# Performance work log

Measured on AMD Instinct MI355X. Metric: run time of the kernel, lower is better.

The kernel has to match this reference:

```python
import jax, jax.numpy as jnp
import numpy as np
from jax import lax

PATCH_SIZE = 14
BLUR_W_L, BLUR_PAD_L, BLUR_REPEATS_L = 5, 2, 5
BLUR_W_U, BLUR_PAD_U, BLUR_REPEATS_U = 7, 3, 3
TOPK_RATIO = 0.001
EPS = 1e-12


def setup_inputs() -> dict:
    key = jax.random.key(0)
    k1, k2, k3, k4 = jax.random.split(key, 4)
    B, N, C = 16, 1024, 768  # 448/14 = 32 -> 32*32 = 1024 patches
    return {
        "middle_patch": jax.random.normal(k1, (B, N, C), dtype=jnp.float32),
        "last_patch": jax.random.normal(k2, (B, N, C), dtype=jnp.float32),
        "predicted_middle_patch": jax.random.normal(k3, (B, N, C), dtype=jnp.float32),
        "predicted_last_patch": jax.random.normal(k4, (B, N, C), dtype=jnp.float32),
        "out_h": 448,
        "out_w": 448,
    }


def _l2_normalize(x):
    # matches torch F.normalize(dim=-1): x / max(||x||_2, 1e-12)
    n = jnp.sqrt(jnp.sum(x * x, axis=-1, keepdims=True))
    return x / jnp.maximum(n, EPS)


def _conv_blur(x, k, pad):
    # x: (B,1,H,W); uniform kxk box filter, stride 1, same-size output
    w = jnp.full((1, 1, k, k), 1.0 / (k * k), dtype=x.dtype)
    return lax.conv_general_dilated(
        x, w, window_strides=(1, 1), padding=[(pad, pad), (pad, pad)],
        dimension_numbers=("NCHW", "OIHW", "NCHW"))


def _blur(x):
    for _ in range(BLUR_REPEATS_L):
        x = _conv_blur(x, BLUR_W_L, BLUR_PAD_L)
    for _ in range(BLUR_REPEATS_U):
        x = _conv_blur(x, BLUR_W_U, BLUR_PAD_U)
    return x


def reference(middle_patch, last_patch, predicted_middle_patch,
              predicted_last_patch, out_h, out_w):
    b = middle_patch.shape[0]
    h, w = int(out_h), int(out_w)
    h_p, w_p = h // PATCH_SIZE, w // PATCH_SIZE

    middle_anom = jnp.sqrt(jnp.sum(
        (_l2_normalize(predicted_middle_patch) - _l2_normalize(middle_patch)) ** 2, axis=-1))
    last_anom = jnp.sqrt(jnp.sum(
        (_l2_normalize(predicted_last_patch) - _l2_normalize(last_patch)) ** 2, axis=-1))
    combined = middle_anom * last_anom  # (B, h_p*w_p)

    anomaly_map = combined.reshape(b, 1, h_p, w_p)
    # bilinear upsample with half-pixel centers == torch align_corners=False
    anomaly_map = jax.image.resize(anomaly_map, (b, 1, h, w), method="bilinear")
    anomaly_map = _blur(anomaly_map)

    n = h * w
    k = max(1, int(n * TOPK_RATIO))
    topk_vals, _ = lax.top_k(anomaly_map.reshape(b, n), k)
    pred_score = jnp.mean(topk_vals, axis=1)
    return anomaly_map, pred_score
```

## Files before the change

### kernel.cpp

```cpp
#include <hip/hip_runtime.h>

constexpr int C = 768;
constexpr int NPATCH = 1024;
constexpr int H = 448, W = 448;
constexpr int HW = H * W;
constexpr int TOPK = 200;
constexpr float EPS = 1e-12f;

constexpr int HBITS = 13;
constexpr int HBINS = 1 << HBITS;
constexpr int HSHIFT = 18;
constexpr int CSTRIDE = 64;

typedef float f32x4 __attribute__((ext_vector_type(4)));

__device__ __forceinline__ float dotv(const f32x4 a, const f32x4 b) {
    return a.x * b.x + a.y * b.y + a.z * b.z + a.w * b.w;
}

__global__ __launch_bounds__(256, 4) void anom_kernel(
    const float* __restrict__ m, const float* __restrict__ l,
    const float* __restrict__ pm, const float* __restrict__ pl,
    float* __restrict__ combined, int rows) {
    int wid = (int)((blockIdx.x * blockDim.x + threadIdx.x) >> 6);
    int lane = threadIdx.x & 63;
    if (wid >= rows) return;
    size_t base = (size_t)wid * C;
    const f32x4* A = (const f32x4*)(m + base);
    const f32x4* B = (const f32x4*)(pm + base);
    const f32x4* Cc = (const f32x4*)(l + base);
    const f32x4* D = (const f32x4*)(pl + base);

    f32x4 a0 = __builtin_nontemporal_load(A + lane);
    f32x4 a1 = __builtin_nontemporal_load(A + lane + 64);
    f32x4 a2 = __builtin_nontemporal_load(A + lane + 128);
    f32x4 b0 = __builtin_nontemporal_load(B + lane);
    f32x4 b1 = __builtin_nontemporal_load(B + lane + 64);
    f32x4 b2 = __builtin_nontemporal_load(B + lane + 128);
    f32x4 c0 = __builtin_nontemporal_load(Cc + lane);
    f32x4 c1 = __builtin_nontemporal_load(Cc + lane + 64);
    f32x4 c2 = __builtin_nontemporal_load(Cc + lane + 128);
    f32x4 d0 = __builtin_nontemporal_load(D + lane);
    f32x4 d1 = __builtin_nontemporal_load(D + lane + 64);
    f32x4 d2 = __builtin_nontemporal_load(D + lane + 128);

    float mm = dotv(a0, a0) + dotv(a1, a1) + dotv(a2, a2);
    float pp = dotv(b0, b0) + dotv(b1, b1) + dotv(b2, b2);
    float mp = dotv(a0, b0) + dotv(a1, b1) + dotv(a2, b2);
    float ll = dotv(c0, c0) + dotv(c1, c1) + dotv(c2, c2);
    float qq = dotv(d0, d0) + dotv(d1, d1) + dotv(d2, d2);
    float lq = dotv(c0, d0) + dotv(c1, d1) + dotv(c2, d2);

#pragma unroll
    for (int off = 32; off > 0; off >>= 1) {
        mm += __shfl_xor(mm, off);
        pp += __shfl_xor(pp, off);
        mp += __shfl_xor(mp, off);
        ll += __shfl_xor(ll, off);
        qq += __shfl_xor(qq, off);
        lq += __shfl_xor(lq, off);
    }
    if (lane == 0) {
        float rm = 1.0f / fmaxf(sqrtf(mm), EPS);
        float rp = 1.0f / fmaxf(sqrtf(pp), EPS);
        float rl = 1.0f / fmaxf(sqrtf(ll), EPS);
        float rq = 1.0f / fmaxf(sqrtf(qq), EPS);
        float d2m = fmaxf(mm * rm * rm - 2.f * mp * rm * rp + pp * rp * rp, 0.f);
        float d2l = fmaxf(ll * rl * rl - 2.f * lq * rl * rq + qq * rq * rq, 0.f);
        combined[wid] = sqrtf(d2m) * sqrtf(d2l);
    }
}


__global__ __launch_bounds__(512) void init_kernel(float* __restrict__ G,
                                                   uint4* __restrict__ zp,
                                                   int n4) {
    if (blockIdx.x != 0) {
        int i = (blockIdx.x - 1) * 512 + threadIdx.x;
        if (i < n4) zp[i] = make_uint4(0u, 0u, 0u, 0u);
        return;
    }
    __shared__ float g[32][449];
    int tid = threadIdx.x;
    int i = tid & 31;
    int chunk = tid >> 5;
    int x0 = chunk * 28;

#pragma unroll 1
    for (int k = 0; k < 28; ++k) {
        int x = x0 + k;
        float sx = (x + 0.5f) * (1.0f / 14.0f) - 0.5f;
        float f0 = floorf(sx);
        float fx = sx - f0;
        int q0 = (int)f0;
        int q0c = min(max(q0, 0), 31);
        int q1c = min(max(q0 + 1, 0), 31);
        float w = 0.f;
        if (q0c == i) w += 1.0f - fx;
        if (q1c == i) w += fx;
        g[i][x] = w;
    }
    __syncthreads();

#pragma unroll 1
    for (int pass = 0; pass < 8; ++pass) {
        float win[34];
#pragma unroll
        for (int j = 0; j < 34; ++j) {
            int xw = x0 - 3 + j;
            win[j] = (xw >= 0 && xw < 448) ? g[i][xw] : 0.f;
        }
        float out[28];
        if (pass < 5) {
            constexpr float inv5 = 1.0f / 5.0f;
#pragma unroll
            for (int k = 0; k < 28; ++k)
                out[k] = (win[k + 1] + win[k + 2] + win[k + 3] + win[k + 4] +
                          win[k + 5]) * inv5;
        } else {
            constexpr float inv7 = 1.0f / 7.0f;
#pragma unroll
            for (int k = 0; k < 28; ++k)
                out[k] = (win[k] + win[k + 1] + win[k + 2] + win[k + 3] +
                          win[k + 4] + win[k + 5] + win[k + 6]) * inv7;
        }
        __syncthreads();
#pragma unroll
        for (int k = 0; k < 28; ++k) g[i][x0 + k] = out[k];
        __syncthreads();
    }
#pragma unroll
    for (int k = 0; k < 28; ++k) G[(x0 + k) * 32 + i] = g[i][x0 + k];
}

__global__ __launch_bounds__(448) void stageA_kernel(
    const float* __restrict__ comb, const float* __restrict__ G,
    float* __restrict__ T) {
    __shared__ float combT[32][32];
    int b = blockIdx.x;
    int x = threadIdx.x;
    const float* cb = comb + (size_t)b * 1024;
    for (int idx = x; idx < 1024; idx += 448)
        combT[idx & 31][idx >> 5] = cb[idx];

    f32x4 grow[8];
#pragma unroll
    for (int k = 0; k < 8; ++k)
        grow[k] = *(const f32x4*)(G + x * 32 + k * 4);
    f32x4 acc[8];
#pragma unroll
    for (int k = 0; k < 8; ++k) acc[k] = (f32x4){0.f, 0.f, 0.f, 0.f};
    __syncthreads();
#pragma unroll
    for (int j = 0; j < 32; ++j) {
        float w = grow[j >> 2][j & 3];
#pragma unroll
        for (int k = 0; k < 8; ++k) {
            f32x4 c = *(const f32x4*)&combT[j][k * 4];
            acc[k] += c * w;
        }
    }
    float* t = T + ((size_t)b * 448 + x) * 32;
#pragma unroll
    for (int k = 0; k < 8; ++k) *(f32x4*)(t + k * 4) = acc[k];
}

__global__ __launch_bounds__(448) void stageB_kernel(
    const float* __restrict__ T, const float* __restrict__ G,
    float* __restrict__ map, unsigned* __restrict__ hist) {
    __shared__ float gband[28][32];
    __shared__ unsigned lh[HBINS];
    int b = blockIdx.x >> 4;
    int band = blockIdx.x & 15;
    int x = threadIdx.x;

    for (int i = x; i < HBINS; i += 448) lh[i] = 0;
    for (int i = x; i < 28 * 32; i += 448)
        gband[i >> 5][i & 31] = G[(band * 28 + (i >> 5)) * 32 + (i & 31)];
    f32x4 t[8];
    const float* tp = T + ((size_t)b * 448 + x) * 32;
#pragma unroll
    for (int k = 0; k < 8; ++k) t[k] = *(const f32x4*)(tp + k * 4);
    __syncthreads();

    float* out = map + (size_t)b * HW + (size_t)band * 28 * W;
#pragma unroll 1
    for (int yy = 0; yy < 28; ++yy) {
        f32x4 a = {0.f, 0.f, 0.f, 0.f};
#pragma unroll
        for (int k = 0; k < 8; ++k) {
            f32x4 g4 = *(const f32x4*)&gband[yy][k * 4];
            a += g4 * t[k];
        }
        float v = a.x + a.y + a.z + a.w;
        out[yy * W + x] = v;
        atomicAdd(&lh[__float_as_uint(v) >> HSHIFT], 1u);
    }
    __syncthreads();
    unsigned* gh = hist + (size_t)b * HBINS;
    for (int i = x; i < HBINS; i += 448) {
        unsigned c = lh[i];
        if (c) atomicAdd(&gh[i], c);
    }
}


__global__ __launch_bounds__(256) void select_kernel(
    const unsigned* __restrict__ hist, int* __restrict__ selbin) {
    int b = blockIdx.x;
    const unsigned* gh = hist + (size_t)b * HBINS;
    constexpr int CHUNK = HBINS / 256;
    __shared__ unsigned ss[257];
    __shared__ unsigned cs2[33];
    __shared__ int sh_base, sh_k;
    int tid = threadIdx.x;
    unsigned s = 0;
#pragma unroll
    for (int j = 0; j < CHUNK; ++j) s += gh[tid * CHUNK + j];
    ss[tid] = s;
    if (tid == 0) ss[256] = 0;
    __syncthreads();
#pragma unroll
    for (int st = 1; st < 256; st <<= 1) {
        unsigned add = (tid + st < 256) ? ss[tid + st] : 0u;
        __syncthreads();
        ss[tid] += add;
        __syncthreads();
    }
    if ((int)ss[tid] >= TOPK && (int)ss[tid + 1] < TOPK) {
        sh_base = tid * CHUNK;
        sh_k = TOPK - (int)ss[tid + 1];
    }
    __syncthreads();
    int base = sh_base, kk = sh_k;
    if (tid < 32) cs2[tid] = gh[base + tid];
    if (tid == 0) cs2[32] = 0;
    __syncthreads();
#pragma unroll
    for (int st = 1; st < 32; st <<= 1) {
        unsigned add = (tid < 32 && tid + st < 32) ? cs2[tid + st] : 0u;
        __syncthreads();
        if (tid < 32) cs2[tid] += add;
        __syncthreads();
    }
    if (tid < 32 && (int)cs2[tid] >= kk && (int)cs2[tid + 1] < kk)
        selbin[b * CSTRIDE] = base + tid;
}

__global__ __launch_bounds__(256) void compact_kernel(
    const float* __restrict__ map, const int* __restrict__ selbin,
    int* __restrict__ ccount, float* __restrict__ cand) {
    int tid = threadIdx.x;
    size_t base = (size_t)blockIdx.x * 1024;
    int b = (int)(base / HW);
    int sb = selbin[b * CSTRIDE];
    const uint4* u4 = (const uint4*)(((const unsigned*)map) + base);
    uint4 v = u4[tid];
    unsigned take0 = ((int)(v.x >> HSHIFT) >= sb);
    unsigned take1 = ((int)(v.y >> HSHIFT) >= sb);
    unsigned take2 = ((int)(v.z >> HSHIFT) >= sb);
    unsigned take3 = ((int)(v.w >> HSHIFT) >= sb);
    int c = (int)(take0 + take1 + take2 + take3);

    __shared__ int blkcnt, blkbase;
    if (tid == 0) blkcnt = 0;
    __syncthreads();
    int pos = 0;
    if (c) pos = atomicAdd(&blkcnt, c);
    __syncthreads();
    if (tid == 0 && blkcnt > 0)
        blkbase = atomicAdd(&ccount[b * CSTRIDE], blkcnt);
    __syncthreads();
    if (c) {
        float* o = cand + (size_t)b * HW + blkbase + pos;
        if (take0) *o++ = __uint_as_float(v.x);
        if (take1) *o++ = __uint_as_float(v.y);
        if (take2) *o++ = __uint_as_float(v.z);
        if (take3) *o = __uint_as_float(v.w);
    }
}

__global__ __launch_bounds__(256) void topk_kernel(
    const float* __restrict__ cand, const int* __restrict__ ccount,
    float* __restrict__ score) {
    int b = blockIdx.x;
    const float* s = cand + (size_t)b * HW;
    const unsigned* u = (const unsigned*)s;
    int M = ccount[b * CSTRIDE];
    __shared__ unsigned hist[256];
    __shared__ unsigned ss[257];
    __shared__ unsigned sh_prefix;
    __shared__ int sh_k;
    int tid = threadIdx.x;

    unsigned prefix = 0;
    int k = TOPK;
    for (int dgt = 3; dgt >= 0; --dgt) {
        hist[tid] = 0;
        __syncthreads();
        for (int i = tid; i < M; i += 256) {
            unsigned v = u[i];
            bool match = (dgt == 3) || ((v >> (8 * (dgt + 1))) == prefix);
            if (match) atomicAdd(&hist[(v >> (8 * dgt)) & 255u], 1u);
        }
        __syncthreads();
        ss[tid] = hist[tid];
        if (tid == 0) ss[256] = 0;
        __syncthreads();
#pragma unroll
        for (int st = 1; st < 256; st <<= 1) {
            unsigned add = (tid + st < 256) ? ss[tid + st] : 0u;
            __syncthreads();
            ss[tid] += add;
            __syncthreads();
        }
        if ((int)ss[tid] >= k && (int)ss[tid + 1] < k) {
            sh_prefix = (prefix << 8) | (unsigned)tid;
            sh_k = k - (int)ss[tid + 1];
        }
        __syncthreads();
        prefix = sh_prefix;
        k = sh_k;
        __syncthreads();
    }

    float thr = __uint_as_float(prefix);
    float sum = 0.f;
    int cnt = 0;
    for (int i = tid; i < M; i += 256) {
        float v = s[i];
        if (v > thr) { sum += v; cnt++; }
    }
#pragma unroll
    for (int off = 32; off > 0; off >>= 1) {
        sum += __shfl_xor(sum, off);
        cnt += __shfl_xor(cnt, off);
    }
    __shared__ float wsum[4];
    __shared__ int wcnt[4];
    int wv = tid >> 6;
    if ((tid & 63) == 0) { wsum[wv] = sum; wcnt[wv] = cnt; }
    __syncthreads();
    if (tid == 0) {
        float s2 = 0.f;
        int c2 = 0;
        for (int i = 0; i < 4; ++i) { s2 += wsum[i]; c2 += wcnt[i]; }
        score[b] = (s2 + (float)(TOPK - c2) * thr) * (1.0f / TOPK);
    }
}

extern "C" void kernel_launch(void* const* d_in, const int* in_sizes, int n_in,
                              void* d_out, int out_size, void* d_ws, size_t ws_size,
                              hipStream_t stream) {
    const float* mid = (const float*)d_in[0];
    const float* last = (const float*)d_in[1];
    const float* pmid = (const float*)d_in[2];
    const float* plast = (const float*)d_in[3];
    int B = in_sizes[0] / (NPATCH * C);

    float* out_map = (float*)d_out;
    float* out_score = out_map + (size_t)B * HW;

    float* combined = (float*)d_ws;
    int* meta = (int*)((char*)d_ws + 64 * 1024);
    int* ccount = meta;
    int* selbin = meta + 16 * CSTRIDE;
    unsigned* hist = (unsigned*)((char*)d_ws + 72 * 1024);
    float* Gw = (float*)((char*)d_ws + 584 * 1024);
    float* Tw = (float*)((char*)d_ws + 644 * 1024);
    float* cand = (float*)((char*)d_ws + 1540 * 1024);

    int n4 = (520 * 1024) / 16;
    init_kernel<<<1 + (n4 + 511) / 512, 512, 0, stream>>>(
        Gw, (uint4*)((char*)d_ws + 64 * 1024), n4);

    int rows = B * NPATCH;
    anom_kernel<<<(rows + 3) / 4, 256, 0, stream>>>(mid, last, pmid, plast,
                                                    combined, rows);

    stageA_kernel<<<B, 448, 0, stream>>>(combined, Gw, Tw);
    stageB_kernel<<<B * 16, 448, 0, stream>>>(Tw, Gw, out_map, hist);

    select_kernel<<<B, 256, 0, stream>>>(hist, selbin);
    int nc = (B * HW) / 1024;
    compact_kernel<<<nc, 256, 0, stream>>>(out_map, selbin, ccount, cand);
    topk_kernel<<<B, 256, 0, stream>>>(cand, ccount, out_score);
}
```

Baseline: 100.6 us.

## Fuse init, select and top-k kernels into neighbours via last-block-done counters

```diff
diff --git a/kernel.cpp b/kernel.cpp
--- a/kernel.cpp
+++ b/kernel.cpp
@@ -11,6 +11,7 @@
 constexpr int HBINS = 1 << HBITS;
 constexpr int HSHIFT = 18;
 constexpr int CSTRIDE = 64;
+constexpr int CBLK = HW / 1024;
 
 typedef float f32x4 __attribute__((ext_vector_type(4)));
 
@@ -21,7 +22,11 @@
 __global__ __launch_bounds__(256, 4) void anom_kernel(
     const float* __restrict__ m, const float* __restrict__ l,
     const float* __restrict__ pm, const float* __restrict__ pl,
-    float* __restrict__ combined, int rows) {
+    float* __restrict__ combined, uint4* __restrict__ zp, int n4, int rows) {
+    if (blockIdx.x < 132) {
+        int z = blockIdx.x * 256 + threadIdx.x;
+        if (z < n4) zp[z] = make_uint4(0u, 0u, 0u, 0u);
+    }
     int wid = (int)((blockIdx.x * blockDim.x + threadIdx.x) >> 6);
     int lane = threadIdx.x & 63;
     if (wid >= rows) return;
@@ -72,22 +77,13 @@
 }
 
 
-__global__ __launch_bounds__(512) void init_kernel(float* __restrict__ G,
-                                                   uint4* __restrict__ zp,
-                                                   int n4) {
-    if (blockIdx.x != 0) {
-        int i = (blockIdx.x - 1) * 512 + threadIdx.x;
-        if (i < n4) zp[i] = make_uint4(0u, 0u, 0u, 0u);
-        return;
-    }
-    __shared__ float g[32][449];
-    int tid = threadIdx.x;
+__device__ void build_G(float (*g)[449], int tid) {
     int i = tid & 31;
     int chunk = tid >> 5;
-    int x0 = chunk * 28;
+    int x0 = chunk * 32;
 
 #pragma unroll 1
-    for (int k = 0; k < 28; ++k) {
+    for (int k = 0; k < 32; ++k) {
         int x = x0 + k;
         float sx = (x + 0.5f) * (1.0f / 14.0f) - 0.5f;
         float f0 = floorf(sx);
@@ -104,38 +100,37 @@
 
 #pragma unroll 1
     for (int pass = 0; pass < 8; ++pass) {
-        float win[34];
-#pragma unroll
-        for (int j = 0; j < 34; ++j) {
+        float win[38];
+#pragma unroll
+        for (int j = 0; j < 38; ++j) {
             int xw = x0 - 3 + j;
             win[j] = (xw >= 0 && xw < 448) ? g[i][xw] : 0.f;
         }
-        float out[28];
+        float out[32];
         if (pass < 5) {
             constexpr float inv5 = 1.0f / 5.0f;
 #pragma unroll
-            for (int k = 0; k < 28; ++k)
+            for (int k = 0; k < 32; ++k)
                 out[k] = (win[k + 1] + win[k + 2] + win[k + 3] + win[k + 4] +
                           win[k + 5]) * inv5;
         } else {
             constexpr float inv7 = 1.0f / 7.0f;
 #pragma unroll
-            for (int k = 0; k < 28; ++k)
+            for (int k = 0; k < 32; ++k)
                 out[k] = (win[k] + win[k + 1] + win[k + 2] + win[k + 3] +
                           win[k + 4] + win[k + 5] + win[k + 6]) * inv7;
         }
         __syncthreads();
 #pragma unroll
-        for (int k = 0; k < 28; ++k) g[i][x0 + k] = out[k];
-        __syncthreads();
-    }
-#pragma unroll
-    for (int k = 0; k < 28; ++k) G[(x0 + k) * 32 + i] = g[i][x0 + k];
+        for (int k = 0; k < 32; ++k) g[i][x0 + k] = out[k];
+        __syncthreads();
+    }
 }
 
 __global__ __launch_bounds__(448) void stageA_kernel(
-    const float* __restrict__ comb, const float* __restrict__ G,
+    const float* __restrict__ comb, float* __restrict__ Gout,
     float* __restrict__ T) {
+    __shared__ float g[32][449];
     __shared__ float combT[32][32];
     int b = blockIdx.x;
     int x = threadIdx.x;
@@ -143,17 +138,14 @@
     for (int idx = x; idx < 1024; idx += 448)
         combT[idx & 31][idx >> 5] = cb[idx];
 
-    f32x4 grow[8];
-#pragma unroll
-    for (int k = 0; k < 8; ++k)
-        grow[k] = *(const f32x4*)(G + x * 32 + k * 4);
+    build_G(g, x);
+
     f32x4 acc[8];
 #pragma unroll
     for (int k = 0; k < 8; ++k) acc[k] = (f32x4){0.f, 0.f, 0.f, 0.f};
-    __syncthreads();
-#pragma unroll
+#pragma unroll 1
     for (int j = 0; j < 32; ++j) {
-        float w = grow[j >> 2][j & 3];
+        float w = g[j][x];
 #pragma unroll
         for (int k = 0; k < 8; ++k) {
             f32x4 c = *(const f32x4*)&combT[j][k * 4];
@@ -163,13 +155,20 @@
     float* t = T + ((size_t)b * 448 + x) * 32;
 #pragma unroll
     for (int k = 0; k < 8; ++k) *(f32x4*)(t + k * 4) = acc[k];
+
+    if (b == 0) {
+        for (int idx = x; idx < 448 * 32; idx += 448)
+            Gout[idx] = g[idx & 31][idx >> 5];
+    }
 }
 
 __global__ __launch_bounds__(448) void stageB_kernel(
     const float* __restrict__ T, const float* __restrict__ G,
-    float* __restrict__ map, unsigned* __restrict__ hist) {
+    float* __restrict__ map, unsigned* __restrict__ hist,
+    int* __restrict__ done, int* __restrict__ selbin) {
     __shared__ float gband[28][32];
     __shared__ unsigned lh[HBINS];
+    __shared__ int is_last;
     int b = blockIdx.x >> 4;
     int band = blockIdx.x & 15;
     int x = threadIdx.x;
@@ -202,54 +201,56 @@
         unsigned c = lh[i];
         if (c) atomicAdd(&gh[i], c);
     }
-}
-
-
-__global__ __launch_bounds__(256) void select_kernel(
-    const unsigned* __restrict__ hist, int* __restrict__ selbin) {
-    int b = blockIdx.x;
-    const unsigned* gh = hist + (size_t)b * HBINS;
-    constexpr int CHUNK = HBINS / 256;
+
+    __threadfence();
+    __syncthreads();
+    if (x == 0) is_last = (atomicAdd(&done[b * CSTRIDE], 1) == 15);
+    __syncthreads();
+    if (!is_last) return;
+    __threadfence();
+
     __shared__ unsigned ss[257];
     __shared__ unsigned cs2[33];
     __shared__ int sh_base, sh_k;
-    int tid = threadIdx.x;
-    unsigned s = 0;
-#pragma unroll
-    for (int j = 0; j < CHUNK; ++j) s += gh[tid * CHUNK + j];
-    ss[tid] = s;
-    if (tid == 0) ss[256] = 0;
+    if (x < 256) {
+        unsigned s = 0;
+#pragma unroll
+        for (int j = 0; j < 32; ++j) s += gh[x * 32 + j];
+        ss[x] = s;
+        if (x == 0) ss[256] = 0;
+    }
     __syncthreads();
 #pragma unroll
     for (int st = 1; st < 256; st <<= 1) {
-        unsigned add = (tid + st < 256) ? ss[tid + st] : 0u;
-        __syncthreads();
-        ss[tid] += add;
-        __syncthreads();
-    }
-    if ((int)ss[tid] >= TOPK && (int)ss[tid + 1] < TOPK) {
-        sh_base = tid * CHUNK;
-        sh_k = TOPK - (int)ss[tid + 1];
+        unsigned add = (x < 256 && x + st < 256) ? ss[x + st] : 0u;
+        __syncthreads();
+        if (x < 256) ss[x] += add;
+        __syncthreads();
+    }
+    if (x < 256 && (int)ss[x] >= TOPK && (int)ss[x + 1] < TOPK) {
+        sh_base = x * 32;
+        sh_k = TOPK - (int)ss[x + 1];
     }
     __syncthreads();
     int base = sh_base, kk = sh_k;
-    if (tid < 32) cs2[tid] = gh[base + tid];
-    if (tid == 0) cs2[32] = 0;
+    if (x < 32) cs2[x] = gh[base + x];
+    if (x == 0) cs2[32] = 0;
     __syncthreads();
 #pragma unroll
     for (int st = 1; st < 32; st <<= 1) {
-        unsigned add = (tid < 32 && tid + st < 32) ? cs2[tid + st] : 0u;
-        __syncthreads();
-        if (tid < 32) cs2[tid] += add;
-        __syncthreads();
-    }
-    if (tid < 32 && (int)cs2[tid] >= kk && (int)cs2[tid + 1] < kk)
-        selbin[b * CSTRIDE] = base + tid;
-}
-
-__global__ __launch_bounds__(256) void compact_kernel(
+        unsigned add = (x < 32 && x + st < 32) ? cs2[x + st] : 0u;
+        __syncthreads();
+        if (x < 32) cs2[x] += add;
+        __syncthreads();
+    }
+    if (x < 32 && (int)cs2[x] >= kk && (int)cs2[x + 1] < kk)
+        selbin[b * CSTRIDE] = base + x;
+}
+
+__global__ __launch_bounds__(256) void compact_topk_kernel(
     const float* __restrict__ map, const int* __restrict__ selbin,
-    int* __restrict__ ccount, float* __restrict__ cand) {
+    int* __restrict__ ccount, int* __restrict__ done2,
+    float* __restrict__ cand, float* __restrict__ score) {
     int tid = threadIdx.x;
     size_t base = (size_t)blockIdx.x * 1024;
     int b = (int)(base / HW);
@@ -262,7 +263,7 @@
     unsigned take3 = ((int)(v.w >> HSHIFT) >= sb);
     int c = (int)(take0 + take1 + take2 + take3);
 
-    __shared__ int blkcnt, blkbase;
+    __shared__ int blkcnt, blkbase, is_last;
     if (tid == 0) blkcnt = 0;
     __syncthreads();
     int pos = 0;
@@ -278,12 +279,14 @@
         if (take2) *o++ = __uint_as_float(v.z);
         if (take3) *o = __uint_as_float(v.w);
     }
-}
-
-__global__ __launch_bounds__(256) void topk_kernel(
-    const float* __restrict__ cand, const int* __restrict__ ccount,
-    float* __restrict__ score) {
-    int b = blockIdx.x;
+
+    __threadfence();
+    __syncthreads();
+    if (tid == 0) is_last = (atomicAdd(&done2[b * CSTRIDE], 1) == CBLK - 1);
+    __syncthreads();
+    if (!is_last) return;
+    __threadfence();
+
     const float* s = cand + (size_t)b * HW;
     const unsigned* u = (const unsigned*)s;
     int M = ccount[b * CSTRIDE];
@@ -291,7 +294,6 @@
     __shared__ unsigned ss[257];
     __shared__ unsigned sh_prefix;
     __shared__ int sh_k;
-    int tid = threadIdx.x;
 
     unsigned prefix = 0;
     int k = TOPK;
@@ -299,9 +301,9 @@
         hist[tid] = 0;
         __syncthreads();
         for (int i = tid; i < M; i += 256) {
-            unsigned v = u[i];
-            bool match = (dgt == 3) || ((v >> (8 * (dgt + 1))) == prefix);
-            if (match) atomicAdd(&hist[(v >> (8 * dgt)) & 255u], 1u);
+            unsigned vv = u[i];
+            bool match = (dgt == 3) || ((vv >> (8 * (dgt + 1))) == prefix);
+            if (match) atomicAdd(&hist[(vv >> (8 * dgt)) & 255u], 1u);
         }
         __syncthreads();
         ss[tid] = hist[tid];
@@ -328,8 +330,8 @@
     float sum = 0.f;
     int cnt = 0;
     for (int i = tid; i < M; i += 256) {
-        float v = s[i];
-        if (v > thr) { sum += v; cnt++; }
+        float vv = s[i];
+        if (vv > thr) { sum += vv; cnt++; }
     }
 #pragma unroll
     for (int off = 32; off > 0; off >>= 1) {
@@ -364,25 +366,23 @@
     float* combined = (float*)d_ws;
     int* meta = (int*)((char*)d_ws + 64 * 1024);
     int* ccount = meta;
-    int* selbin = meta + 16 * CSTRIDE;
-    unsigned* hist = (unsigned*)((char*)d_ws + 72 * 1024);
-    float* Gw = (float*)((char*)d_ws + 584 * 1024);
-    float* Tw = (float*)((char*)d_ws + 644 * 1024);
-    float* cand = (float*)((char*)d_ws + 1540 * 1024);
-
-    int n4 = (520 * 1024) / 16;
-    init_kernel<<<1 + (n4 + 511) / 512, 512, 0, stream>>>(
-        Gw, (uint4*)((char*)d_ws + 64 * 1024), n4);
+    int* selbin = meta + 1024;
+    int* done = meta + 2048;
+    int* done2 = meta + 3072;
+    unsigned* hist = (unsigned*)((char*)d_ws + 80 * 1024);
+    float* Gw = (float*)((char*)d_ws + 592 * 1024);
+    float* Tw = (float*)((char*)d_ws + 652 * 1024);
+    float* cand = (float*)((char*)d_ws + 1548 * 1024);
 
     int rows = B * NPATCH;
-    anom_kernel<<<(rows + 3) / 4, 256, 0, stream>>>(mid, last, pmid, plast,
-                                                    combined, rows);
+    int n4 = (528 * 1024) / 16;
+    anom_kernel<<<(rows + 3) / 4, 256, 0, stream>>>(
+        mid, last, pmid, plast, combined,
+        (uint4*)((char*)d_ws + 64 * 1024), n4, rows);
 
     stageA_kernel<<<B, 448, 0, stream>>>(combined, Gw, Tw);
-    stageB_kernel<<<B * 16, 448, 0, stream>>>(Tw, Gw, out_map, hist);
-
-    select_kernel<<<B, 256, 0, stream>>>(hist, selbin);
-    int nc = (B * HW) / 1024;
-    compact_kernel<<<nc, 256, 0, stream>>>(out_map, selbin, ccount, cand);
-    topk_kernel<<<B, 256, 0, stream>>>(cand, ccount, out_score);
-}
+    stageB_kernel<<<B * 16, 448, 0, stream>>>(Tw, Gw, out_map, hist, done,
+                                              selbin);
+    compact_topk_kernel<<<B * CBLK, 256, 0, stream>>>(out_map, selbin, ccount,
+                                                      done2, cand, out_score);
+}
```

After: 324.1 us. 3.22x slower.

## Fold init kernel into anom and stageA kernels to drop a launch

Applied to the files above, without the earlier changes.

```diff
diff --git a/kernel.cpp b/kernel.cpp
--- a/kernel.cpp
+++ b/kernel.cpp
@@ -21,7 +21,11 @@
 __global__ __launch_bounds__(256, 4) void anom_kernel(
     const float* __restrict__ m, const float* __restrict__ l,
     const float* __restrict__ pm, const float* __restrict__ pl,
-    float* __restrict__ combined, int rows) {
+    float* __restrict__ combined, uint4* __restrict__ zp, int n4, int rows) {
+    if (blockIdx.x < 132) {
+        int z = blockIdx.x * 256 + threadIdx.x;
+        if (z < n4) zp[z] = make_uint4(0u, 0u, 0u, 0u);
+    }
     int wid = (int)((blockIdx.x * blockDim.x + threadIdx.x) >> 6);
     int lane = threadIdx.x & 63;
     if (wid >= rows) return;
@@ -72,22 +76,13 @@
 }
 
 
-__global__ __launch_bounds__(512) void init_kernel(float* __restrict__ G,
-                                                   uint4* __restrict__ zp,
-                                                   int n4) {
-    if (blockIdx.x != 0) {
-        int i = (blockIdx.x - 1) * 512 + threadIdx.x;
-        if (i < n4) zp[i] = make_uint4(0u, 0u, 0u, 0u);
-        return;
-    }
-    __shared__ float g[32][449];
-    int tid = threadIdx.x;
+__device__ void build_G(float (*g)[449], int tid) {
     int i = tid & 31;
     int chunk = tid >> 5;
-    int x0 = chunk * 28;
+    int x0 = chunk * 32;
 
 #pragma unroll 1
-    for (int k = 0; k < 28; ++k) {
+    for (int k = 0; k < 32; ++k) {
         int x = x0 + k;
         float sx = (x + 0.5f) * (1.0f / 14.0f) - 0.5f;
         float f0 = floorf(sx);
@@ -104,38 +99,37 @@
 
 #pragma unroll 1
     for (int pass = 0; pass < 8; ++pass) {
-        float win[34];
-#pragma unroll
-        for (int j = 0; j < 34; ++j) {
+        float win[38];
+#pragma unroll
+        for (int j = 0; j < 38; ++j) {
             int xw = x0 - 3 + j;
             win[j] = (xw >= 0 && xw < 448) ? g[i][xw] : 0.f;
         }
-        float out[28];
+        float out[32];
         if (pass < 5) {
             constexpr float inv5 = 1.0f / 5.0f;
 #pragma unroll
-            for (int k = 0; k < 28; ++k)
+            for (int k = 0; k < 32; ++k)
                 out[k] = (win[k + 1] + win[k + 2] + win[k + 3] + win[k + 4] +
                           win[k + 5]) * inv5;
         } else {
             constexpr float inv7 = 1.0f / 7.0f;
 #pragma unroll
-            for (int k = 0; k < 28; ++k)
+            for (int k = 0; k < 32; ++k)
                 out[k] = (win[k] + win[k + 1] + win[k + 2] + win[k + 3] +
                           win[k + 4] + win[k + 5] + win[k + 6]) * inv7;
         }
         __syncthreads();
 #pragma unroll
-        for (int k = 0; k < 28; ++k) g[i][x0 + k] = out[k];
-        __syncthreads();
-    }
-#pragma unroll
-    for (int k = 0; k < 28; ++k) G[(x0 + k) * 32 + i] = g[i][x0 + k];
+        for (int k = 0; k < 32; ++k) g[i][x0 + k] = out[k];
+        __syncthreads();
+    }
 }
 
 __global__ __launch_bounds__(448) void stageA_kernel(
-    const float* __restrict__ comb, const float* __restrict__ G,
+    const float* __restrict__ comb, float* __restrict__ Gout,
     float* __restrict__ T) {
+    __shared__ float g[32][449];
     __shared__ float combT[32][32];
     int b = blockIdx.x;
     int x = threadIdx.x;
@@ -143,17 +137,14 @@
     for (int idx = x; idx < 1024; idx += 448)
         combT[idx & 31][idx >> 5] = cb[idx];
 
-    f32x4 grow[8];
-#pragma unroll
-    for (int k = 0; k < 8; ++k)
-        grow[k] = *(const f32x4*)(G + x * 32 + k * 4);
+    build_G(g, x);
+
     f32x4 acc[8];
 #pragma unroll
     for (int k = 0; k < 8; ++k) acc[k] = (f32x4){0.f, 0.f, 0.f, 0.f};
-    __syncthreads();
-#pragma unroll
+#pragma unroll 1
     for (int j = 0; j < 32; ++j) {
-        float w = grow[j >> 2][j & 3];
+        float w = g[j][x];
 #pragma unroll
         for (int k = 0; k < 8; ++k) {
             f32x4 c = *(const f32x4*)&combT[j][k * 4];
@@ -163,6 +154,11 @@
     float* t = T + ((size_t)b * 448 + x) * 32;
 #pragma unroll
     for (int k = 0; k < 8; ++k) *(f32x4*)(t + k * 4) = acc[k];
+
+    if (b == 0) {
+        for (int idx = x; idx < 448 * 32; idx += 448)
+            Gout[idx] = g[idx & 31][idx >> 5];
+    }
 }
 
 __global__ __launch_bounds__(448) void stageB_kernel(
@@ -364,19 +360,17 @@
     float* combined = (float*)d_ws;
     int* meta = (int*)((char*)d_ws + 64 * 1024);
     int* ccount = meta;
-    int* selbin = meta + 16 * CSTRIDE;
-    unsigned* hist = (unsigned*)((char*)d_ws + 72 * 1024);
-    float* Gw = (float*)((char*)d_ws + 584 * 1024);
-    float* Tw = (float*)((char*)d_ws + 644 * 1024);
-    float* cand = (float*)((char*)d_ws + 1540 * 1024);
-
-    int n4 = (520 * 1024) / 16;
-    init_kernel<<<1 + (n4 + 511) / 512, 512, 0, stream>>>(
-        Gw, (uint4*)((char*)d_ws + 64 * 1024), n4);
+    int* selbin = meta + 1024;
+    unsigned* hist = (unsigned*)((char*)d_ws + 80 * 1024);
+    float* Gw = (float*)((char*)d_ws + 592 * 1024);
+    float* Tw = (float*)((char*)d_ws + 652 * 1024);
+    float* cand = (float*)((char*)d_ws + 1548 * 1024);
 
     int rows = B * NPATCH;
-    anom_kernel<<<(rows + 3) / 4, 256, 0, stream>>>(mid, last, pmid, plast,
-                                                    combined, rows);
+    int n4 = (528 * 1024) / 16;
+    anom_kernel<<<(rows + 3) / 4, 256, 0, stream>>>(
+        mid, last, pmid, plast, combined,
+        (uint4*)((char*)d_ws + 64 * 1024), n4, rows);
 
     stageA_kernel<<<B, 448, 0, stream>>>(combined, Gw, Tw);
     stageB_kernel<<<B * 16, 448, 0, stream>>>(Tw, Gw, out_map, hist);
```

Measured after the change: 100.3 us. No clear change (-0.3%).
